# Performance work log

Hardware: AMD Instinct MI355X
Metric: run time of the kernel (lower is better)

Reference implementation:

```python
import jax, jax.numpy as jnp
import numpy as np

B = 1048576
H = 256


def _parity_W():
    # W[i,j,k] = 1 if (i+j+k+1) % 2 == 0  <=>  (i+j+k) odd
    idx = jnp.arange(2)
    s = idx[:, None, None] + idx[None, :, None] + idx[None, None, :]
    return (s % 2 == 1).astype(jnp.float32)


def setup_inputs() -> dict:
    key = jax.random.key(0)
    ks = jax.random.split(key, 7)
    x = jax.random.normal(ks[0], (B, 3), dtype=jnp.float32)
    w1 = jax.random.normal(ks[1], (H, 3), dtype=jnp.float32) * (1.0 / np.sqrt(3))
    b1 = jax.random.normal(ks[2], (H,), dtype=jnp.float32) * 0.01
    w2 = jax.random.normal(ks[3], (H, H), dtype=jnp.float32) * (1.0 / np.sqrt(H))
    b2 = jax.random.normal(ks[4], (H,), dtype=jnp.float32) * 0.01
    w3 = jax.random.normal(ks[5], (3, H), dtype=jnp.float32) * (1.0 / np.sqrt(H))
    b3 = jax.random.normal(ks[6], (3,), dtype=jnp.float32) * 0.01
    return {"x": x, "w1": w1, "b1": b1, "w2": w2, "b2": b2, "w3": w3, "b3": b3}


def reference(x, w1, b1, w2, b2, w3, b3):
    # MLP: 3 -> H -> H -> 3 with ReLU
    h = jax.nn.relu(x @ w1.T + b1)          # (B, H)
    h = jax.nn.relu(h @ w2.T + b2)          # (B, H)
    logitC = h @ w3.T + b3                  # (B, 3)

    eps = 1e-05
    sig = jax.nn.sigmoid(logitC)            # (B, 3)
    p_pos = (sig + eps) / (1.0 + 2.0 * eps)
    p_neg = (1.0 - sig + eps) / (1.0 + 2.0 * eps)
    p = jnp.stack([p_neg, p_pos], axis=-1)  # (B, 3, 2): per-concept Bernoulli probs

    W = _parity_W()                          # (2, 2, 2) XOR-parity indicator
    pred1 = jnp.einsum('bi,bj,bk,ijk->b', p[:, 0], p[:, 1], p[:, 2], W)  # (B,)
    pred = jnp.stack([1.0 - pred1, pred1], axis=1)  # (B, 2)
    pred = (pred + 0.001) / (1.0 + 2.0 * 0.001)
    return pred, logitC
```

## Files before the change

kernel.cpp:

```cpp
#include <hip/hip_runtime.h>

typedef _Float16 f16;
typedef _Float16 f16x8 __attribute__((ext_vector_type(8)));
typedef float f32x16 __attribute__((ext_vector_type(16)));
typedef unsigned int u32;
typedef unsigned int u32x4 __attribute__((ext_vector_type(4)));

#define THREADS 512
#define MTILE   128
#define NBLK    256

#define H1_OFF   0
#define XS_OFF   65536
#define W1P_OFF  114688
#define PART_OFF 118784
#define LDS_BYTES 131072

__global__ __launch_bounds__(THREADS, 1)
void fused_mlp_parity(const float* __restrict__ x,
                      const float* __restrict__ w1,
                      const float* __restrict__ b1,
                      const float* __restrict__ w2,
                      const float* __restrict__ b2,
                      const float* __restrict__ w3,
                      const float* __restrict__ b3,
                      float* __restrict__ out, int Bsz) {
  __shared__ __align__(128) unsigned char lds[LDS_BYTES];
  const int tid  = threadIdx.x;
  const int lane = tid & 63;
  const int wave = tid >> 6;
  const int arow = lane & 31;
  const int half = lane >> 5;

  float* part = (float*)(lds + PART_OFF);

  const int ntiles = Bsz / MTILE;
  const int tpb    = ntiles / NBLK;
  const int t0     = blockIdx.x * tpb;

  {
    const float4* xg = (const float4*)(x + (size_t)t0 * (MTILE*3));
    float4* xv = (float4*)(lds + XS_OFF);
    const int n4 = tpb * (MTILE*3/4);
    for (int i = tid; i < n4; i += THREADS) xv[i] = xg[i];
  }
  for (int i = tid; i < 256; i += THREADS) {
    float2 lo; lo.x = w1[i*3+0]; lo.y = w1[i*3+1];
    float2 hi; hi.x = w1[i*3+2]; hi.y = b1[i];
    const u32 key = ((u32)(i >> 3) & 15) << 3;
    *(float2*)(lds + W1P_OFF + (((u32)i*16)     ^ key)) = lo;
    *(float2*)(lds + W1P_OFF + (((u32)i*16 + 8) ^ key)) = hi;
  }

  f16x8 w2A[16];
  {
    const int col = (wave << 5) + arow;
#pragma unroll
    for (int ks = 0; ks < 16; ++ks) {
      const float* src = w2 + (size_t)col*256 + ks*16 + half*8;
      float4 u0 = *(const float4*)src;
      float4 u1 = *(const float4*)(src + 4);
      f16x8 v;
      v[0]=(f16)u0.x; v[1]=(f16)u0.y; v[2]=(f16)u0.z; v[3]=(f16)u0.w;
      v[4]=(f16)u1.x; v[5]=(f16)u1.y; v[6]=(f16)u1.z; v[7]=(f16)u1.w;
      w2A[ks] = v;
    }
  }
  f16x8 b2A = {};  if (half == 0) b2A[0] = (f16)b2[(wave<<5) + arow];
  f16x8 ones = {}; if (half == 0) ones[0] = (f16)1.0f;
  f16x8 w3A[2];
#pragma unroll
  for (int q = 0; q < 2; ++q) {
    f16x8 v = {};
    if (arow < 3) {
#pragma unroll
      for (int j = 0; j < 8; ++j)
        v[j] = (f16)w3[arow*256 + (wave<<5) + q*16 + half*8 + j];
    }
    w3A[q] = v;
  }
  const float b3r0 = b3[0], b3r1 = b3[1], b3r2 = b3[2];
  const size_t outL = (size_t)Bsz * 2;

  __syncthreads();

  for (int tl = 0; tl < tpb; ++tl) {
    const size_t base = ((size_t)t0 + tl) * MTILE;

    {
      const int hb = tid & 31;
      const int rg = tid >> 5;
      const float* xs = (const float*)(lds + XS_OFF) + (u32)tl * (MTILE*3);
      const u32 wk = ((u32)hb & 15) << 3;
      float4 wv[8];
#pragma unroll
      for (int i = 0; i < 8; ++i) {
        const int h = hb*8 + i;
        float2 a = *(const float2*)(lds + W1P_OFF + (((u32)h*16)     ^ wk));
        float2 b = *(const float2*)(lds + W1P_OFF + (((u32)h*16 + 8) ^ wk));
        wv[i].x = a.x; wv[i].y = a.y; wv[i].z = b.x; wv[i].w = b.y;
      }
#pragma unroll
      for (int rr = 0; rr < 8; ++rr) {
        const int r = rg*8 + rr;
        const float x0 = xs[r*3+0], x1 = xs[r*3+1], x2 = xs[r*3+2];
        f16x8 ah;
#pragma unroll
        for (int i = 0; i < 8; ++i) {
          float v = fmaf(x2, wv[i].z, fmaf(x1, wv[i].y, fmaf(x0, wv[i].x, wv[i].w)));
          ah[i] = (f16)fmaxf(v, 0.0f);
        }
        *(f16x8*)(lds + H1_OFF + ((u32)r << 9)
                  + ((((u32)hb) << 4) ^ ((((u32)r) & 15) << 4))) = ah;
      }
    }
    __syncthreads();

    f32x16 acc[4];
#pragma unroll
    for (int nt = 0; nt < 4; ++nt) {
      f32x16 z = {};
      acc[nt] = __builtin_amdgcn_mfma_f32_32x32x16_f16(b2A, ones, z, 0,0,0);
    }
    {
      const u32 rk = ((u32)(arow & 15)) << 4;
      const u32 cb = (u32)half << 4;
#pragma unroll
      for (int ks = 0; ks < 16; ++ks) {
        f16x8 fr[4];
#pragma unroll
        for (int nt = 0; nt < 4; ++nt)
          fr[nt] = *(const f16x8*)(lds + H1_OFF + ((u32)(nt*32 + arow) << 9)
                                   + (((((u32)ks) << 5) + cb) ^ rk));
#pragma unroll
        for (int nt = 0; nt < 4; ++nt)
          acc[nt] = __builtin_amdgcn_mfma_f32_32x32x16_f16(w2A[ks], fr[nt], acc[nt], 0,0,0);
      }
    }

#pragma unroll
    for (int nt = 0; nt < 4; ++nt) {
      f32x16 a3 = {};
#pragma unroll
      for (int q = 0; q < 2; ++q) {
        const int i0 = q*8;
        const float c0 = fmaxf(acc[nt][i0+0], 0.f), c1 = fmaxf(acc[nt][i0+1], 0.f);
        const float c2 = fmaxf(acc[nt][i0+2], 0.f), c3 = fmaxf(acc[nt][i0+3], 0.f);
        const float c4 = fmaxf(acc[nt][i0+4], 0.f), c5 = fmaxf(acc[nt][i0+5], 0.f);
        const float c6 = fmaxf(acc[nt][i0+6], 0.f), c7 = fmaxf(acc[nt][i0+7], 0.f);
        u32 P = __builtin_bit_cast(u32, __builtin_amdgcn_cvt_pkrtz(c0, c1));
        u32 Q = __builtin_bit_cast(u32, __builtin_amdgcn_cvt_pkrtz(c2, c3));
        u32 R = __builtin_bit_cast(u32, __builtin_amdgcn_cvt_pkrtz(c4, c5));
        u32 S = __builtin_bit_cast(u32, __builtin_amdgcn_cvt_pkrtz(c6, c7));
        asm("v_permlane32_swap_b32 %0, %1" : "+v"(P), "+v"(R));
        asm("v_permlane32_swap_b32 %0, %1" : "+v"(Q), "+v"(S));
        u32x4 w; w[0]=P; w[1]=Q; w[2]=R; w[3]=S;
        a3 = __builtin_amdgcn_mfma_f32_32x32x16_f16(w3A[q], __builtin_bit_cast(f16x8, w), a3, 0,0,0);
      }
      if (half == 0) {
        float* pr = part + (u32)wave*384 + (u32)(nt*32 + arow)*3;
        pr[0] = a3[0]; pr[1] = a3[1]; pr[2] = a3[2];
      }
    }
    __syncthreads();

    if (tid < MTILE) {
      const int r = tid;
      float l0 = b3r0, l1 = b3r1, l2 = b3r2;
#pragma unroll
      for (int w8 = 0; w8 < 8; ++w8) {
        const float* pr = part + (u32)w8*384 + (u32)r*3;
        l0 += pr[0]; l1 += pr[1]; l2 += pr[2];
      }
      const float inv1p2e = 1.0f / (1.0f + 2.0f * 1e-5f);
      const float tt0 = (1.0f - 2.0f / (1.0f + __expf(-l0))) * inv1p2e;
      const float tt1 = (1.0f - 2.0f / (1.0f + __expf(-l1))) * inv1p2e;
      const float tt2 = (1.0f - 2.0f / (1.0f + __expf(-l2))) * inv1p2e;
      const float pred1 = 0.5f * (1.0f - tt0 * tt1 * tt2);
      const size_t grow = base + (size_t)r;
      float2 ov;
      ov.x = (1.0f - pred1 + 0.001f) * (1.0f / 1.002f);
      ov.y = (pred1 + 0.001f) * (1.0f / 1.002f);
      *(float2*)(out + grow*2) = ov;
      out[outL + grow*3 + 0] = l0;
      out[outL + grow*3 + 1] = l1;
      out[outL + grow*3 + 2] = l2;
    }
  }
}

extern "C" void kernel_launch(void* const* d_in, const int* in_sizes, int n_in,
                              void* d_out, int out_size, void* d_ws, size_t ws_size,
                              hipStream_t stream) {
  const float* x  = (const float*)d_in[0];
  const float* w1 = (const float*)d_in[1];
  const float* b1 = (const float*)d_in[2];
  const float* w2 = (const float*)d_in[3];
  const float* b2 = (const float*)d_in[4];
  const float* w3 = (const float*)d_in[5];
  const float* b3 = (const float*)d_in[6];
  float* out = (float*)d_out;
  const int Bsz = in_sizes[0] / 3;

  dim3 grid(NBLK), block(THREADS);
  fused_mlp_parity<<<grid, block, 0, stream>>>(x, w1, b1, w2, b2, w3, b3, out, Bsz);
}
```

Baseline: 228.7 us.

## Pipeline MLP tiles with double-buffered layer-1 MFMA and deferred epilogue

Moves the first layer from scalar FMAs onto MFMA, with bias folded in through a ones column. The hidden activations are double-buffered in LDS, so the next tile's layer 1 is produced while the current tile finishes, and the per-tile barriers drop from three to one. Waves are re-split into a 4x2 grid (64 output columns by 64 rows each), which halves the partial-sum reduction but doubles the w2 fragments held in registers. The x tiles are now prefetched two tiles ahead instead of all staged at the start, and the final sigmoid/parity epilogue lags one tile behind. The x staging index expression looks odd (96 + tid-192+96), and layer-1 inputs drop to fp16, both of which risk correctness.

```diff
diff --git a/kernel.cpp b/kernel.cpp
--- a/kernel.cpp
+++ b/kernel.cpp
@@ -11,10 +11,9 @@
 #define NBLK    256
 
 #define H1_OFF   0
-#define XS_OFF   65536
-#define W1P_OFF  114688
-#define PART_OFF 118784
-#define LDS_BYTES 131072
+#define XS_OFF   131072
+#define PART_OFF 134144
+#define LDS_BYTES 146432
 
 __global__ __launch_bounds__(THREADS, 1)
 void fused_mlp_parity(const float* __restrict__ x,
@@ -31,30 +30,28 @@
   const int wave = tid >> 6;
   const int arow = lane & 31;
   const int half = lane >> 5;
-
-  float* part = (float*)(lds + PART_OFF);
+  const int cw   = wave & 3;
+  const int rw   = wave >> 2;
+  const int mhalf  = cw * 64;
+  const int rowblk = rw * 64;
 
   const int ntiles = Bsz / MTILE;
   const int tpb    = ntiles / NBLK;
   const int t0     = blockIdx.x * tpb;
 
+  float* xsf   = (float*)(lds + XS_OFF);
+  float* partf = (float*)(lds + PART_OFF);
+
   {
-    const float4* xg = (const float4*)(x + (size_t)t0 * (MTILE*3));
-    float4* xv = (float4*)(lds + XS_OFF);
-    const int n4 = tpb * (MTILE*3/4);
-    for (int i = tid; i < n4; i += THREADS) xv[i] = xg[i];
-  }
-  for (int i = tid; i < 256; i += THREADS) {
-    float2 lo; lo.x = w1[i*3+0]; lo.y = w1[i*3+1];
-    float2 hi; hi.x = w1[i*3+2]; hi.y = b1[i];
-    const u32 key = ((u32)(i >> 3) & 15) << 3;
-    *(float2*)(lds + W1P_OFF + (((u32)i*16)     ^ key)) = lo;
-    *(float2*)(lds + W1P_OFF + (((u32)i*16 + 8) ^ key)) = hi;
-  }
-
-  f16x8 w2A[16];
-  {
-    const int col = (wave << 5) + arow;
+    const float4* xg = (const float4*)x;
+    if (tid < 96)       ((float4*)xsf)[tid]       = xg[(size_t)t0*96 + tid];
+    else if (tid < 192) ((float4*)xsf)[96 + tid-192+96] = xg[(size_t)(t0+1)*96 + (tid-96)];
+  }
+
+  f16x8 w2A[2][16];
+#pragma unroll
+  for (int mt = 0; mt < 2; ++mt) {
+    const int col = mhalf + mt*32 + arow;
 #pragma unroll
     for (int ks = 0; ks < 16; ++ks) {
       const float* src = w2 + (size_t)col*256 + ks*16 + half*8;
@@ -63,113 +60,157 @@
       f16x8 v;
       v[0]=(f16)u0.x; v[1]=(f16)u0.y; v[2]=(f16)u0.z; v[3]=(f16)u0.w;
       v[4]=(f16)u1.x; v[5]=(f16)u1.y; v[6]=(f16)u1.z; v[7]=(f16)u1.w;
-      w2A[ks] = v;
-    }
-  }
-  f16x8 b2A = {};  if (half == 0) b2A[0] = (f16)b2[(wave<<5) + arow];
+      w2A[mt][ks] = v;
+    }
+  }
+  f16x8 w1A[2];
+#pragma unroll
+  for (int mt = 0; mt < 2; ++mt) {
+    f16x8 v = {};
+    if (half == 0) {
+      const int col = mhalf + mt*32 + arow;
+      v[0] = (f16)w1[col*3+0]; v[1] = (f16)w1[col*3+1];
+      v[2] = (f16)w1[col*3+2]; v[3] = (f16)b1[col];
+    }
+    w1A[mt] = v;
+  }
+  f16x8 b2A[2];
+#pragma unroll
+  for (int mt = 0; mt < 2; ++mt) {
+    f16x8 v = {};
+    if (half == 0) v[0] = (f16)b2[mhalf + mt*32 + arow];
+    b2A[mt] = v;
+  }
   f16x8 ones = {}; if (half == 0) ones[0] = (f16)1.0f;
-  f16x8 w3A[2];
-#pragma unroll
-  for (int q = 0; q < 2; ++q) {
-    f16x8 v = {};
-    if (arow < 3) {
-#pragma unroll
-      for (int j = 0; j < 8; ++j)
-        v[j] = (f16)w3[arow*256 + (wave<<5) + q*16 + half*8 + j];
-    }
-    w3A[q] = v;
-  }
+  f16x8 w3A[2][2];
+#pragma unroll
+  for (int mt = 0; mt < 2; ++mt)
+#pragma unroll
+    for (int q = 0; q < 2; ++q) {
+      f16x8 v = {};
+      if (arow < 3) {
+#pragma unroll
+        for (int j = 0; j < 8; ++j)
+          v[j] = (f16)w3[arow*256 + mhalf + mt*32 + q*16 + half*8 + j];
+      }
+      w3A[mt][q] = v;
+    }
   const float b3r0 = b3[0], b3r1 = b3[1], b3r2 = b3[2];
   const size_t outL = (size_t)Bsz * 2;
+  const u32 rk = ((u32)(arow & 15)) << 4;
+
+  auto PHASE_B = [&](int buf) {
+    unsigned char* h1b = lds + H1_OFF + (u32)buf*65536;
+    const float* xb_src = xsf + (u32)buf*384;
+#pragma unroll
+    for (int nt = 0; nt < 2; ++nt) {
+      const int r = rowblk + nt*32 + arow;
+      f16x8 xb = {};
+      if (half == 0) {
+        const float* xr = xb_src + r*3;
+        xb[0] = (f16)xr[0]; xb[1] = (f16)xr[1]; xb[2] = (f16)xr[2];
+        xb[3] = (f16)1.0f;
+      }
+#pragma unroll
+      for (int mt = 0; mt < 2; ++mt) {
+        f32x16 h = {};
+        h = __builtin_amdgcn_mfma_f32_32x32x16_f16(w1A[mt], xb, h, 0,0,0);
+#pragma unroll
+        for (int q = 0; q < 2; ++q) {
+          const int i0 = q*8;
+          const float c0 = fmaxf(h[i0+0], 0.f), c1 = fmaxf(h[i0+1], 0.f);
+          const float c2 = fmaxf(h[i0+2], 0.f), c3 = fmaxf(h[i0+3], 0.f);
+          const float c4 = fmaxf(h[i0+4], 0.f), c5 = fmaxf(h[i0+5], 0.f);
+          const float c6 = fmaxf(h[i0+6], 0.f), c7 = fmaxf(h[i0+7], 0.f);
+          u32 P = __builtin_bit_cast(u32, __builtin_amdgcn_cvt_pkrtz(c0, c1));
+          u32 Q = __builtin_bit_cast(u32, __builtin_amdgcn_cvt_pkrtz(c2, c3));
+          u32 R = __builtin_bit_cast(u32, __builtin_amdgcn_cvt_pkrtz(c4, c5));
+          u32 S = __builtin_bit_cast(u32, __builtin_amdgcn_cvt_pkrtz(c6, c7));
+          asm("v_permlane32_swap_b32 %0, %1" : "+v"(P), "+v"(R));
+          asm("v_permlane32_swap_b32 %0, %1" : "+v"(Q), "+v"(S));
+          u32x4 w; w[0]=P; w[1]=Q; w[2]=R; w[3]=S;
+          const u32 slot = (u32)((mhalf + mt*32 + q*16)*2 + half*16);
+          *(u32x4*)(h1b + ((u32)r << 9) + (slot ^ rk)) = w;
+        }
+      }
+    }
+  };
 
   __syncthreads();
+  PHASE_B(0);
+  __syncthreads();
 
   for (int tl = 0; tl < tpb; ++tl) {
-    const size_t base = ((size_t)t0 + tl) * MTILE;
-
+    const int cur = tl & 1, nxt = cur ^ 1;
+
+    f32x16 acc[2][2];
+#pragma unroll
+    for (int mt = 0; mt < 2; ++mt)
+#pragma unroll
+      for (int nt = 0; nt < 2; ++nt) {
+        f32x16 z = {};
+        acc[mt][nt] = __builtin_amdgcn_mfma_f32_32x32x16_f16(b2A[mt], ones, z, 0,0,0);
+      }
     {
-      const int hb = tid & 31;
-      const int rg = tid >> 5;
-      const float* xs = (const float*)(lds + XS_OFF) + (u32)tl * (MTILE*3);
-      const u32 wk = ((u32)hb & 15) << 3;
-      float4 wv[8];
-#pragma unroll
-      for (int i = 0; i < 8; ++i) {
-        const int h = hb*8 + i;
-        float2 a = *(const float2*)(lds + W1P_OFF + (((u32)h*16)     ^ wk));
-        float2 b = *(const float2*)(lds + W1P_OFF + (((u32)h*16 + 8) ^ wk));
-        wv[i].x = a.x; wv[i].y = a.y; wv[i].z = b.x; wv[i].w = b.y;
-      }
-#pragma unroll
-      for (int rr = 0; rr < 8; ++rr) {
-        const int r = rg*8 + rr;
-        const float x0 = xs[r*3+0], x1 = xs[r*3+1], x2 = xs[r*3+2];
-        f16x8 ah;
-#pragma unroll
-        for (int i = 0; i < 8; ++i) {
-          float v = fmaf(x2, wv[i].z, fmaf(x1, wv[i].y, fmaf(x0, wv[i].x, wv[i].w)));
-          ah[i] = (f16)fmaxf(v, 0.0f);
+      const unsigned char* h1b = lds + H1_OFF + (u32)cur*65536;
+      const u32 cb = (u32)half << 4;
+#pragma unroll
+      for (int ks = 0; ks < 16; ++ks) {
+        f16x8 fr[2];
+#pragma unroll
+        for (int nt = 0; nt < 2; ++nt)
+          fr[nt] = *(const f16x8*)(h1b + ((u32)(rowblk + nt*32 + arow) << 9)
+                                   + (((((u32)ks) << 5) + cb) ^ rk));
+#pragma unroll
+        for (int mt = 0; mt < 2; ++mt)
+#pragma unroll
+          for (int nt = 0; nt < 2; ++nt)
+            acc[mt][nt] = __builtin_amdgcn_mfma_f32_32x32x16_f16(w2A[mt][ks], fr[nt], acc[mt][nt], 0,0,0);
+      }
+    }
+
+#pragma unroll
+    for (int nt = 0; nt < 2; ++nt) {
+      f32x16 a3 = {};
+#pragma unroll
+      for (int mt = 0; mt < 2; ++mt)
+#pragma unroll
+        for (int q = 0; q < 2; ++q) {
+          const int i0 = q*8;
+          const float c0 = fmaxf(acc[mt][nt][i0+0], 0.f), c1 = fmaxf(acc[mt][nt][i0+1], 0.f);
+          const float c2 = fmaxf(acc[mt][nt][i0+2], 0.f), c3 = fmaxf(acc[mt][nt][i0+3], 0.f);
+          const float c4 = fmaxf(acc[mt][nt][i0+4], 0.f), c5 = fmaxf(acc[mt][nt][i0+5], 0.f);
+          const float c6 = fmaxf(acc[mt][nt][i0+6], 0.f), c7 = fmaxf(acc[mt][nt][i0+7], 0.f);
+          u32 P = __builtin_bit_cast(u32, __builtin_amdgcn_cvt_pkrtz(c0, c1));
+          u32 Q = __builtin_bit_cast(u32, __builtin_amdgcn_cvt_pkrtz(c2, c3));
+          u32 R = __builtin_bit_cast(u32, __builtin_amdgcn_cvt_pkrtz(c4, c5));
+          u32 S = __builtin_bit_cast(u32, __builtin_amdgcn_cvt_pkrtz(c6, c7));
+          asm("v_permlane32_swap_b32 %0, %1" : "+v"(P), "+v"(R));
+          asm("v_permlane32_swap_b32 %0, %1" : "+v"(Q), "+v"(S));
+          u32x4 w; w[0]=P; w[1]=Q; w[2]=R; w[3]=S;
+          a3 = __builtin_amdgcn_mfma_f32_32x32x16_f16(w3A[mt][q], __builtin_bit_cast(f16x8, w), a3, 0,0,0);
         }
-        *(f16x8*)(lds + H1_OFF + ((u32)r << 9)
-                  + ((((u32)hb) << 4) ^ ((((u32)r) & 15) << 4))) = ah;
-      }
-    }
-    __syncthreads();
-
-    f32x16 acc[4];
-#pragma unroll
-    for (int nt = 0; nt < 4; ++nt) {
-      f32x16 z = {};
-      acc[nt] = __builtin_amdgcn_mfma_f32_32x32x16_f16(b2A, ones, z, 0,0,0);
-    }
-    {
-      const u32 rk = ((u32)(arow & 15)) << 4;
-      const u32 cb = (u32)half << 4;
-#pragma unroll
-      for (int ks = 0; ks < 16; ++ks) {
-        f16x8 fr[4];
-#pragma unroll
-        for (int nt = 0; nt < 4; ++nt)
-          fr[nt] = *(const f16x8*)(lds + H1_OFF + ((u32)(nt*32 + arow) << 9)
-                                   + (((((u32)ks) << 5) + cb) ^ rk));
-#pragma unroll
-        for (int nt = 0; nt < 4; ++nt)
-          acc[nt] = __builtin_amdgcn_mfma_f32_32x32x16_f16(w2A[ks], fr[nt], acc[nt], 0,0,0);
-      }
-    }
-
-#pragma unroll
-    for (int nt = 0; nt < 4; ++nt) {
-      f32x16 a3 = {};
-#pragma unroll
-      for (int q = 0; q < 2; ++q) {
-        const int i0 = q*8;
-        const float c0 = fmaxf(acc[nt][i0+0], 0.f), c1 = fmaxf(acc[nt][i0+1], 0.f);
-        const float c2 = fmaxf(acc[nt][i0+2], 0.f), c3 = fmaxf(acc[nt][i0+3], 0.f);
-        const float c4 = fmaxf(acc[nt][i0+4], 0.f), c5 = fmaxf(acc[nt][i0+5], 0.f);
-        const float c6 = fmaxf(acc[nt][i0+6], 0.f), c7 = fmaxf(acc[nt][i0+7], 0.f);
-        u32 P = __builtin_bit_cast(u32, __builtin_amdgcn_cvt_pkrtz(c0, c1));
-        u32 Q = __builtin_bit_cast(u32, __builtin_amdgcn_cvt_pkrtz(c2, c3));
-        u32 R = __builtin_bit_cast(u32, __builtin_amdgcn_cvt_pkrtz(c4, c5));
-        u32 S = __builtin_bit_cast(u32, __builtin_amdgcn_cvt_pkrtz(c6, c7));
-        asm("v_permlane32_swap_b32 %0, %1" : "+v"(P), "+v"(R));
-        asm("v_permlane32_swap_b32 %0, %1" : "+v"(Q), "+v"(S));
-        u32x4 w; w[0]=P; w[1]=Q; w[2]=R; w[3]=S;
-        a3 = __builtin_amdgcn_mfma_f32_32x32x16_f16(w3A[q], __builtin_bit_cast(f16x8, w), a3, 0,0,0);
-      }
       if (half == 0) {
-        float* pr = part + (u32)wave*384 + (u32)(nt*32 + arow)*3;
+        float* pr = partf + (u32)cur*1536 + (u32)(cw*128 + rowblk + nt*32 + arow)*3;
         pr[0] = a3[0]; pr[1] = a3[1]; pr[2] = a3[2];
       }
     }
-    __syncthreads();
-
-    if (tid < MTILE) {
+
+    if (tl + 1 < tpb) PHASE_B(nxt);
+
+    if (tl + 2 < tpb && tid >= 416) {
+      const int i = tid - 416;
+      ((float4*)(xsf + (u32)cur*384))[i] =
+          ((const float4*)x)[(size_t)(t0 + tl + 2)*96 + i];
+    }
+
+    if (tl > 0 && tid < MTILE) {
       const int r = tid;
+      const float* pb = partf + (u32)nxt*1536;
       float l0 = b3r0, l1 = b3r1, l2 = b3r2;
 #pragma unroll
-      for (int w8 = 0; w8 < 8; ++w8) {
-        const float* pr = part + (u32)w8*384 + (u32)r*3;
+      for (int c4 = 0; c4 < 4; ++c4) {
+        const float* pr = pb + (u32)(c4*128 + r)*3;
         l0 += pr[0]; l1 += pr[1]; l2 += pr[2];
       }
       const float inv1p2e = 1.0f / (1.0f + 2.0f * 1e-5f);
@@ -177,7 +218,7 @@
       const float tt1 = (1.0f - 2.0f / (1.0f + __expf(-l1))) * inv1p2e;
       const float tt2 = (1.0f - 2.0f / (1.0f + __expf(-l2))) * inv1p2e;
       const float pred1 = 0.5f * (1.0f - tt0 * tt1 * tt2);
-      const size_t grow = base + (size_t)r;
+      const size_t grow = (size_t)(t0 + tl - 1)*MTILE + r;
       float2 ov;
       ov.x = (1.0f - pred1 + 0.001f) * (1.0f / 1.002f);
       ov.y = (pred1 + 0.001f) * (1.0f / 1.002f);
@@ -186,6 +227,31 @@
       out[outL + grow*3 + 1] = l1;
       out[outL + grow*3 + 2] = l2;
     }
+    __syncthreads();
+  }
+
+  if (tid < MTILE) {
+    const int r = tid;
+    const float* pb = partf + (u32)((tpb - 1) & 1)*1536;
+    float l0 = b3r0, l1 = b3r1, l2 = b3r2;
+#pragma unroll
+    for (int c4 = 0; c4 < 4; ++c4) {
+      const float* pr = pb + (u32)(c4*128 + r)*3;
+      l0 += pr[0]; l1 += pr[1]; l2 += pr[2];
+    }
+    const float inv1p2e = 1.0f / (1.0f + 2.0f * 1e-5f);
+    const float tt0 = (1.0f - 2.0f / (1.0f + __expf(-l0))) * inv1p2e;
+    const float tt1 = (1.0f - 2.0f / (1.0f + __expf(-l1))) * inv1p2e;
+    const float tt2 = (1.0f - 2.0f / (1.0f + __expf(-l2))) * inv1p2e;
+    const float pred1 = 0.5f * (1.0f - tt0 * tt1 * tt2);
+    const size_t grow = (size_t)(t0 + tpb - 1)*MTILE + r;
+    float2 ov;
+    ov.x = (1.0f - pred1 + 0.001f) * (1.0f / 1.002f);
+    ov.y = (pred1 + 0.001f) * (1.0f / 1.002f);
+    *(float2*)(out + grow*2) = ov;
+    out[outL + grow*3 + 0] = l0;
+    out[outL + grow*3 + 1] = l1;
+    out[outL + grow*3 + 2] = l2;
   }
 }
 
```

Result: slower. 264.1 us (+15.5%).
